# Performance work log

Measured on AMD Instinct MI355X. Metric: run time of the kernel, lower is better.

Reference implementation:

```python
import jax, jax.numpy as jnp
import numpy as np
from jax import lax

B, S, I, H = 256, 2048, 32, 18


def setup_inputs() -> dict:
    key = jax.random.key(0)
    ks = jax.random.split(key, 40)
    d = {}
    d['input'] = jax.random.normal(ks[0], (B, S, I), jnp.float32)
    d['hidden'] = jnp.zeros((3, B, H), jnp.float32)
    ki = 1
    sc = 1.0 / np.sqrt(H)
    for l in range(3):
        in_dim = I if l == 0 else H
        d[f'Wih{l}'] = jax.random.uniform(ks[ki], (H, in_dim), jnp.float32, -sc, sc); ki += 1
        d[f'bih{l}'] = jax.random.uniform(ks[ki], (H,), jnp.float32, -sc, sc); ki += 1
        d[f'Whh{l}'] = jax.random.uniform(ks[ki], (H, H), jnp.float32, -sc, sc); ki += 1
        d[f'bhh{l}'] = jax.random.uniform(ks[ki], (H,), jnp.float32, -sc, sc); ki += 1
    dims = [(H, H), (10, H), (8, 10), (4, 8), (2, 4), (1, 2)]
    for i, (o, ii) in enumerate(dims, start=1):
        s = 1.0 / np.sqrt(ii)
        d[f'W{i}'] = jax.random.uniform(ks[ki], (o, ii), jnp.float32, -s, s); ki += 1
        d[f'b{i}'] = jax.random.uniform(ks[ki], (o,), jnp.float32, -s, s); ki += 1
    return d


def _rnn_layer(x, h0, Wih, bih, Whh, bhh):
    # Precompute input contributions for all timesteps (one big GEMM),
    # then scan only the tiny hxh recurrence.
    xW = jnp.einsum('bsi,hi->bsh', x, Wih) + bih + bhh  # [B,S,H]

    def step(h, xw_t):
        h = jnp.tanh(xw_t + h @ Whh.T)
        return h, h

    hT, ys = lax.scan(step, h0, jnp.swapaxes(xW, 0, 1))  # scan over time
    return jnp.swapaxes(ys, 0, 1), hT


def reference(input, hidden,
              Wih0, bih0, Whh0, bhh0,
              Wih1, bih1, Whh1, bhh1,
              Wih2, bih2, Whh2, bhh2,
              W1, b1, W2, b2, W3, b3, W4, b4, W5, b5, W6, b6):
    layer_params = [(Wih0, bih0, Whh0, bhh0),
                    (Wih1, bih1, Whh1, bhh1),
                    (Wih2, bih2, Whh2, bhh2)]
    x = input
    h_finals = []
    for l, (Wih, bih, Whh, bhh) in enumerate(layer_params):
        x, hT = _rnn_layer(x, hidden[l], Wih, bih, Whh, bhh)
        h_finals.append(hT)
    hidden_out = jnp.stack(h_finals)  # [3,B,H]

    b_, s_, h_ = x.shape
    o = x.reshape(-1, h_)
    for W, b in [(W1, b1), (W2, b2), (W3, b3), (W4, b4), (W5, b5)]:
        o = jax.nn.relu(o @ W.T + b)
    o = o @ W6.T + b6
    return o.reshape(b_, s_, -1), hidden_out
```

## Files before the change

kernel.cpp:

```cpp
#include <hip/hip_runtime.h>

#define Bsz 256
#define Ssz 2048
#define Isz 32
#define Hsz 18
#define SCALE 2.885390081777927f

typedef float f2 __attribute__((ext_vector_type(2)));
typedef float f4 __attribute__((ext_vector_type(4)));

#define LO2(v) __builtin_shufflevector(v, v, 0, 1)
#define HI2(v) __builtin_shufflevector(v, v, 2, 3)

__device__ __forceinline__ float exp2_fast(float x) {
#if __has_builtin(__builtin_amdgcn_exp2f)
    return __builtin_amdgcn_exp2f(x);
#else
    return __expf(x * 0.6931471805599453f);
#endif
}

__global__ __launch_bounds__(256) void input_gemm(
    const float* __restrict__ x,
    const float* __restrict__ Wih0,
    const float* __restrict__ bih0,
    const float* __restrict__ bhh0,
    float* __restrict__ xw0T)
{
    __shared__ float xs[256 * 33];
    int blk = blockIdx.x;
    int b = blk >> 3;
    int t0 = (blk & 7) << 8;
    int tid = threadIdx.x;

    const float4* src = (const float4*)(x + ((size_t)b * Ssz + t0) * Isz);
#pragma unroll
    for (int k = 0; k < 8; ++k) {
        int l = k * 256 + tid;
        float4 v = src[l];
        int row = l >> 3, k4 = l & 7;
        float* p = xs + row * 33 + k4 * 4;
        p[0] = v.x; p[1] = v.y; p[2] = v.z; p[3] = v.w;
    }
    __syncthreads();

    float xv[32];
    const float* myrow = xs + tid * 33;
#pragma unroll
    for (int k = 0; k < 32; ++k) xv[k] = myrow[k];

    float* op = xw0T + (size_t)b * (Hsz * Ssz) + (t0 + tid);
#pragma unroll
    for (int ii = 0; ii < Hsz; ++ii) {
        float acc = bih0[ii] + bhh0[ii];
#pragma unroll
        for (int k = 0; k < 32; ++k) acc = fmaf(xv[k], Wih0[ii * Isz + k], acc);
        op[(size_t)ii * Ssz] = acc * SCALE;
    }
}

__global__ __launch_bounds__(64) void rnn_scan(
    const float* __restrict__ xw0T,
    const float* __restrict__ hidden,
    const float* __restrict__ Whh0,
    const float* __restrict__ Wih1, const float* __restrict__ bih1,
    const float* __restrict__ Whh1, const float* __restrict__ bhh1,
    const float* __restrict__ Wih2, const float* __restrict__ bih2,
    const float* __restrict__ Whh2, const float* __restrict__ bhh2,
    float* __restrict__ h2T,
    float* __restrict__ hid_out)
{
    const int b = blockIdx.x;
    const int r = threadIdx.x;
    const int g = (r < 18) ? 0 : (r < 36) ? 1 : (r < 54) ? 2 : 3;
    const int i = r - g * 18;
    const bool lane_active = (g < 3);
    const bool g0lane = (g == 0);
    const bool g2lane = (g == 2);

    __shared__ __align__(16) float sbuf[176];
    for (int k = r; k < 176; k += 64) sbuf[k] = 0.0f;

    float wx[Hsz], wh[Hsz];
    float econst = 0.0f;
    float h = 0.0f;
    if (lane_active) {
        const float* Whh = (g == 0) ? Whh0 : (g == 1) ? Whh1 : Whh2;
#pragma unroll
        for (int j = 0; j < Hsz; ++j) wh[j] = Whh[i * Hsz + j] * SCALE;
        if (g >= 1) {
            const float* Wih = (g == 1) ? Wih1 : Wih2;
            const float* bi  = (g == 1) ? bih1 : bih2;
            const float* bh  = (g == 1) ? bhh1 : bhh2;
#pragma unroll
            for (int j = 0; j < Hsz; ++j) wx[j] = Wih[i * Hsz + j] * SCALE;
            econst = (bi[i] + bh[i]) * SCALE;
        } else {
#pragma unroll
            for (int j = 0; j < Hsz; ++j) wx[j] = 0.0f;
        }
        h = hidden[(g * Bsz + b) * Hsz + i];
    } else {
#pragma unroll
        for (int j = 0; j < Hsz; ++j) { wx[j] = 0.0f; wh[j] = 0.0f; }
    }

    f2 wx2[9], wh2[9];
#pragma unroll
    for (int k = 0; k < 9; ++k) {
        wx2[k] = f2{wx[2 * k], wx[2 * k + 1]};
        wh2[k] = f2{wh[2 * k], wh[2 * k + 1]};
    }

    const int slot  = 36 + 36 * g + i;
    const int xbase = 36 * g;
    const int hbase = 36 * g + 36;

    sbuf[slot] = h;
    __builtin_amdgcn_wave_barrier();

    const float* xwp = xw0T + (size_t)b * (Hsz * Ssz) + (size_t)((g == 0) ? i : 0) * Ssz;
    float*       hop2 = h2T + (size_t)b * (Hsz * Ssz) + (size_t)i * Ssz;

    const f4* sx4 = (const f4*)(sbuf + xbase);
    const f4* sh4 = (const f4*)(sbuf + hbase);
    const f2* sx2 = (const f2*)(sbuf + xbase + 16);
    const f2* sh2 = (const f2*)(sbuf + hbase + 16);

    f4 cur = *(const f4*)(xwp + 0);
    f4 nxt = *(const f4*)(xwp + 4);
    f4 ob;

    auto do_tick = [&](float e, bool dostore, int st) -> float {
        f4 qa = sx4[0], qb = sx4[1], qc = sx4[2], qd = sx4[3];
        f2 qe = sx2[0];
        f4 pa = sh4[0], pb = sh4[1], pc = sh4[2], pd = sh4[3];
        f2 pe = sh2[0];
        if (dostore && g2lane) *(f4*)(hop2 + st) = ob;
        f2 ax0 = f2{e, 0.0f}, ax1 = f2{0.0f, 0.0f}, ax2 = f2{0.0f, 0.0f};
        f2 ah0 = f2{0.0f, 0.0f}, ah1 = f2{0.0f, 0.0f}, ah2 = f2{0.0f, 0.0f};
        ax0 = __builtin_elementwise_fma(wx2[0], LO2(qa), ax0);
        ax1 = __builtin_elementwise_fma(wx2[1], HI2(qa), ax1);
        ax2 = __builtin_elementwise_fma(wx2[2], LO2(qb), ax2);
        ah0 = __builtin_elementwise_fma(wh2[0], LO2(pa), ah0);
        ah1 = __builtin_elementwise_fma(wh2[1], HI2(pa), ah1);
        ah2 = __builtin_elementwise_fma(wh2[2], LO2(pb), ah2);
        ax0 = __builtin_elementwise_fma(wx2[3], HI2(qb), ax0);
        ax1 = __builtin_elementwise_fma(wx2[4], LO2(qc), ax1);
        ax2 = __builtin_elementwise_fma(wx2[5], HI2(qc), ax2);
        ah0 = __builtin_elementwise_fma(wh2[3], HI2(pb), ah0);
        ah1 = __builtin_elementwise_fma(wh2[4], LO2(pc), ah1);
        ah2 = __builtin_elementwise_fma(wh2[5], HI2(pc), ah2);
        ax0 = __builtin_elementwise_fma(wx2[6], LO2(qd), ax0);
        ax1 = __builtin_elementwise_fma(wx2[7], HI2(qd), ax1);
        ax2 = __builtin_elementwise_fma(wx2[8], qe,      ax2);
        ah0 = __builtin_elementwise_fma(wh2[6], LO2(pd), ah0);
        ah1 = __builtin_elementwise_fma(wh2[7], HI2(pd), ah1);
        ah2 = __builtin_elementwise_fma(wh2[8], pe,      ah2);
        f2 t0 = ax0 + ax1, t1 = ax2 + ah0, t2 = ah1 + ah2;
        f2 s = (t0 + t1) + t2;
        float a = s.x + s.y;
        float t = exp2_fast(a);
        return fmaf(-2.0f, __builtin_amdgcn_rcpf(t + 1.0f), 1.0f);
    };

    {
        f4 fut = *(const f4*)(xwp + 8);
        float ev[4] = {cur.x, cur.y, cur.z, cur.w};
#pragma unroll
        for (int u = 0; u < 4; ++u) {
            const int T = u;
            float e = g0lane ? ev[u] : econst;
            float nh = do_tick(e, false, 0);
            bool upd = lane_active && (T >= g);
            h = upd ? nh : h;
            sbuf[slot] = h;
            if (u == 2) ob.x = h; else if (u == 3) ob.y = h;
            __builtin_amdgcn_wave_barrier();
        }
        cur = nxt; nxt = fut;
    }

    for (int tb = 4; tb < Ssz; tb += 4) {
        int tl = tb + 8; if (tl > Ssz - 4) tl = Ssz - 4;
        f4 fut = *(const f4*)(xwp + tl);
        float ev[4] = {cur.x, cur.y, cur.z, cur.w};
#pragma unroll
        for (int u = 0; u < 4; ++u) {
            float e = g0lane ? ev[u] : econst;
            h = do_tick(e, u == 2, tb - 4);
            sbuf[slot] = h;
            if (u == 0) ob.z = h;
            else if (u == 1) ob.w = h;
            else if (u == 2) ob.x = h;
            else ob.y = h;
            __builtin_amdgcn_wave_barrier();
        }
        cur = nxt; nxt = fut;
    }

    {
        float ev[4] = {cur.x, cur.y, cur.z, cur.w};
#pragma unroll
        for (int u = 0; u < 2; ++u) {
            const int T = Ssz + u;
            float e = g0lane ? ev[u] : econst;
            float nh = do_tick(e, false, 0);
            bool upd = lane_active && (T <= Ssz - 1 + g);
            h = upd ? nh : h;
            sbuf[slot] = h;
            if (u == 0) ob.z = h; else ob.w = h;
            __builtin_amdgcn_wave_barrier();
        }
        if (g2lane) *(f4*)(hop2 + Ssz - 4) = ob;
    }

    if (lane_active) hid_out[(g * Bsz + b) * Hsz + i] = h;
}

__global__ __launch_bounds__(256) void mlp_head(
    const float* __restrict__ h2T,
    const float* __restrict__ W1, const float* __restrict__ b1,
    const float* __restrict__ W2, const float* __restrict__ b2,
    const float* __restrict__ W3, const float* __restrict__ b3,
    const float* __restrict__ W4, const float* __restrict__ b4,
    const float* __restrict__ W5, const float* __restrict__ b5,
    const float* __restrict__ W6, const float* __restrict__ b6,
    float* __restrict__ out)
{
    int idx = blockIdx.x * 256 + threadIdx.x;
    int b = idx >> 11;
    int t = idx & (Ssz - 1);
    const float* hp = h2T + (size_t)b * (Hsz * Ssz) + t;
    float v[Hsz];
#pragma unroll
    for (int j = 0; j < Hsz; ++j) v[j] = hp[(size_t)j * Ssz];

    float a1[18];
#pragma unroll
    for (int o = 0; o < 18; ++o) {
        float acc = b1[o];
#pragma unroll
        for (int j = 0; j < 18; ++j) acc = fmaf(W1[o * 18 + j], v[j], acc);
        a1[o] = fmaxf(acc, 0.0f);
    }
    float a2[10];
#pragma unroll
    for (int o = 0; o < 10; ++o) {
        float acc = b2[o];
#pragma unroll
        for (int j = 0; j < 18; ++j) acc = fmaf(W2[o * 18 + j], a1[j], acc);
        a2[o] = fmaxf(acc, 0.0f);
    }
    float a3[8];
#pragma unroll
    for (int o = 0; o < 8; ++o) {
        float acc = b3[o];
#pragma unroll
        for (int j = 0; j < 10; ++j) acc = fmaf(W3[o * 10 + j], a2[j], acc);
        a3[o] = fmaxf(acc, 0.0f);
    }
    float a4[4];
#pragma unroll
    for (int o = 0; o < 4; ++o) {
        float acc = b4[o];
#pragma unroll
        for (int j = 0; j < 8; ++j) acc = fmaf(W4[o * 8 + j], a3[j], acc);
        a4[o] = fmaxf(acc, 0.0f);
    }
    float a5[2];
#pragma unroll
    for (int o = 0; o < 2; ++o) {
        float acc = b5[o];
#pragma unroll
        for (int j = 0; j < 4; ++j) acc = fmaf(W5[o * 4 + j], a4[j], acc);
        a5[o] = fmaxf(acc, 0.0f);
    }
    float r6 = b6[0];
    r6 = fmaf(W6[0], a5[0], r6);
    r6 = fmaf(W6[1], a5[1], r6);
    out[idx] = r6;
}

extern "C" void kernel_launch(void* const* d_in, const int* in_sizes, int n_in,
                              void* d_out, int out_size, void* d_ws, size_t ws_size,
                              hipStream_t stream) {
    (void)in_sizes; (void)n_in; (void)out_size; (void)ws_size;
    const float* input  = (const float*)d_in[0];
    const float* hidden = (const float*)d_in[1];
    const float* Wih0 = (const float*)d_in[2];  const float* bih0 = (const float*)d_in[3];
    const float* Whh0 = (const float*)d_in[4];  const float* bhh0 = (const float*)d_in[5];
    const float* Wih1 = (const float*)d_in[6];  const float* bih1 = (const float*)d_in[7];
    const float* Whh1 = (const float*)d_in[8];  const float* bhh1 = (const float*)d_in[9];
    const float* Wih2 = (const float*)d_in[10]; const float* bih2 = (const float*)d_in[11];
    const float* Whh2 = (const float*)d_in[12]; const float* bhh2 = (const float*)d_in[13];
    const float* W1 = (const float*)d_in[14]; const float* b1 = (const float*)d_in[15];
    const float* W2 = (const float*)d_in[16]; const float* b2 = (const float*)d_in[17];
    const float* W3 = (const float*)d_in[18]; const float* b3 = (const float*)d_in[19];
    const float* W4 = (const float*)d_in[20]; const float* b4 = (const float*)d_in[21];
    const float* W5 = (const float*)d_in[22]; const float* b5 = (const float*)d_in[23];
    const float* W6 = (const float*)d_in[24]; const float* b6 = (const float*)d_in[25];

    float* xw0T = (float*)d_ws;
    float* h2T  = xw0T + (size_t)Bsz * Hsz * Ssz;
    float* out  = (float*)d_out;
    float* hout = out + (size_t)Bsz * Ssz;

    input_gemm<<<dim3(2048), dim3(256), 0, stream>>>(input, Wih0, bih0, bhh0, xw0T);
    rnn_scan<<<dim3(256), dim3(64), 0, stream>>>(xw0T, hidden, Whh0,
                                                 Wih1, bih1, Whh1, bhh1,
                                                 Wih2, bih2, Whh2, bhh2,
                                                 h2T, hout);
    mlp_head<<<dim3(2048), dim3(256), 0, stream>>>(h2T, W1, b1, W2, b2, W3, b3,
                                                   W4, b4, W5, b5, W6, b6, out);
}
```

Measured before the change: 441.3 us.

## Process two batch sequences per wave in RNN scan to interleave recurrences

Each rnn_scan block now advances two independent batch elements in lockstep, with separate shared-memory state buffers and interleaved dot-product/tanh chains, and the grid is halved to 128 blocks. The intent is to hide the per-step LDS and transcendental latency of the serial recurrence with a second independent chain. The cost is more instructions per step and only half as many waves in flight, leaving many CUs idle.

New measurement: 642.5 us. 45.6% more time.

```diff
diff --git a/kernel.cpp b/kernel.cpp
--- a/kernel.cpp
+++ b/kernel.cpp
@@ -70,7 +70,8 @@
     float* __restrict__ h2T,
     float* __restrict__ hid_out)
 {
-    const int b = blockIdx.x;
+    const int bp = blockIdx.x;
+    const int b0 = bp * 2, b1 = b0 + 1;
     const int r = threadIdx.x;
     const int g = (r < 18) ? 0 : (r < 36) ? 1 : (r < 54) ? 2 : 3;
     const int i = r - g * 18;
@@ -78,12 +79,14 @@
     const bool g0lane = (g == 0);
     const bool g2lane = (g == 2);
 
-    __shared__ __align__(16) float sbuf[176];
-    for (int k = r; k < 176; k += 64) sbuf[k] = 0.0f;
+    __shared__ __align__(16) float sbuf[384];
+    for (int k = r; k < 384; k += 64) sbuf[k] = 0.0f;
+    float* sbufA = sbuf;
+    float* sbufB = sbuf + 192;
 
     float wx[Hsz], wh[Hsz];
     float econst = 0.0f;
-    float h = 0.0f;
+    float hA = 0.0f, hB = 0.0f;
     if (lane_active) {
         const float* Whh = (g == 0) ? Whh0 : (g == 1) ? Whh1 : Whh2;
 #pragma unroll
@@ -99,7 +102,8 @@
 #pragma unroll
             for (int j = 0; j < Hsz; ++j) wx[j] = 0.0f;
         }
-        h = hidden[(g * Bsz + b) * Hsz + i];
+        hA = hidden[(g * Bsz + b0) * Hsz + i];
+        hB = hidden[(g * Bsz + b1) * Hsz + i];
     } else {
 #pragma unroll
         for (int j = 0; j < Hsz; ++j) { wx[j] = 0.0f; wh[j] = 0.0f; }
@@ -116,27 +120,30 @@
     const int xbase = 36 * g;
     const int hbase = 36 * g + 36;
 
-    sbuf[slot] = h;
+    sbufA[slot] = hA;
+    sbufB[slot] = hB;
     __builtin_amdgcn_wave_barrier();
 
-    const float* xwp = xw0T + (size_t)b * (Hsz * Ssz) + (size_t)((g == 0) ? i : 0) * Ssz;
-    float*       hop2 = h2T + (size_t)b * (Hsz * Ssz) + (size_t)i * Ssz;
-
-    const f4* sx4 = (const f4*)(sbuf + xbase);
-    const f4* sh4 = (const f4*)(sbuf + hbase);
-    const f2* sx2 = (const f2*)(sbuf + xbase + 16);
-    const f2* sh2 = (const f2*)(sbuf + hbase + 16);
-
-    f4 cur = *(const f4*)(xwp + 0);
-    f4 nxt = *(const f4*)(xwp + 4);
-    f4 ob;
-
-    auto do_tick = [&](float e, bool dostore, int st) -> float {
-        f4 qa = sx4[0], qb = sx4[1], qc = sx4[2], qd = sx4[3];
-        f2 qe = sx2[0];
-        f4 pa = sh4[0], pb = sh4[1], pc = sh4[2], pd = sh4[3];
-        f2 pe = sh2[0];
-        if (dostore && g2lane) *(f4*)(hop2 + st) = ob;
+    const float* xwpA = xw0T + (size_t)b0 * (Hsz * Ssz) + (size_t)((g == 0) ? i : 0) * Ssz;
+    const float* xwpB = xw0T + (size_t)b1 * (Hsz * Ssz) + (size_t)((g == 0) ? i : 0) * Ssz;
+    float*       hopA = h2T + (size_t)b0 * (Hsz * Ssz) + (size_t)i * Ssz;
+    float*       hopB = h2T + (size_t)b1 * (Hsz * Ssz) + (size_t)i * Ssz;
+
+    const f4* sx4A = (const f4*)(sbufA + xbase);
+    const f4* sh4A = (const f4*)(sbufA + hbase);
+    const f2* sx2A = (const f2*)(sbufA + xbase + 16);
+    const f2* sh2A = (const f2*)(sbufA + hbase + 16);
+    const f4* sx4B = (const f4*)(sbufB + xbase);
+    const f4* sh4B = (const f4*)(sbufB + hbase);
+    const f2* sx2B = (const f2*)(sbufB + xbase + 16);
+    const f2* sh2B = (const f2*)(sbufB + hbase + 16);
+
+    f4 curA = *(const f4*)(xwpA + 0), nxtA = *(const f4*)(xwpA + 4);
+    f4 curB = *(const f4*)(xwpB + 0), nxtB = *(const f4*)(xwpB + 4);
+    f4 obA, obB;
+
+    auto dot_tanh = [&](float e, f4 qa, f4 qb, f4 qc, f4 qd, f2 qe,
+                                 f4 pa, f4 pb, f4 pc, f4 pd, f2 pe) -> float {
         f2 ax0 = f2{e, 0.0f}, ax1 = f2{0.0f, 0.0f}, ax2 = f2{0.0f, 0.0f};
         f2 ah0 = f2{0.0f, 0.0f}, ah1 = f2{0.0f, 0.0f}, ah2 = f2{0.0f, 0.0f};
         ax0 = __builtin_elementwise_fma(wx2[0], LO2(qa), ax0);
@@ -164,58 +171,91 @@
         return fmaf(-2.0f, __builtin_amdgcn_rcpf(t + 1.0f), 1.0f);
     };
 
+    auto do_tick = [&](float eA, float eB, bool use_mask, bool upd,
+                       bool dostore, int st) {
+        f4 qa0 = sx4A[0], qb0 = sx4A[1], qc0 = sx4A[2], qd0 = sx4A[3];
+        f2 qe0 = sx2A[0];
+        f4 pa0 = sh4A[0], pb0 = sh4A[1], pc0 = sh4A[2], pd0 = sh4A[3];
+        f2 pe0 = sh2A[0];
+        f4 qa1 = sx4B[0], qb1 = sx4B[1], qc1 = sx4B[2], qd1 = sx4B[3];
+        f2 qe1 = sx2B[0];
+        f4 pa1 = sh4B[0], pb1 = sh4B[1], pc1 = sh4B[2], pd1 = sh4B[3];
+        f2 pe1 = sh2B[0];
+        if (dostore && g2lane) {
+            *(f4*)(hopA + st) = obA;
+            *(f4*)(hopB + st) = obB;
+        }
+        float nhA = dot_tanh(eA, qa0, qb0, qc0, qd0, qe0, pa0, pb0, pc0, pd0, pe0);
+        hA = use_mask ? (upd ? nhA : hA) : nhA;
+        sbufA[slot] = hA;
+        float nhB = dot_tanh(eB, qa1, qb1, qc1, qd1, qe1, pa1, pb1, pc1, pd1, pe1);
+        hB = use_mask ? (upd ? nhB : hB) : nhB;
+        sbufB[slot] = hB;
+        __builtin_amdgcn_wave_barrier();
+    };
+
     {
-        f4 fut = *(const f4*)(xwp + 8);
-        float ev[4] = {cur.x, cur.y, cur.z, cur.w};
+        f4 futA = *(const f4*)(xwpA + 8);
+        f4 futB = *(const f4*)(xwpB + 8);
+        float evA[4] = {curA.x, curA.y, curA.z, curA.w};
+        float evB[4] = {curB.x, curB.y, curB.z, curB.w};
 #pragma unroll
         for (int u = 0; u < 4; ++u) {
             const int T = u;
-            float e = g0lane ? ev[u] : econst;
-            float nh = do_tick(e, false, 0);
+            float eA = g0lane ? evA[u] : econst;
+            float eB = g0lane ? evB[u] : econst;
             bool upd = lane_active && (T >= g);
-            h = upd ? nh : h;
-            sbuf[slot] = h;
-            if (u == 2) ob.x = h; else if (u == 3) ob.y = h;
-            __builtin_amdgcn_wave_barrier();
-        }
-        cur = nxt; nxt = fut;
+            do_tick(eA, eB, true, upd, false, 0);
+            if (u == 2) { obA.x = hA; obB.x = hB; }
+            else if (u == 3) { obA.y = hA; obB.y = hB; }
+        }
+        curA = nxtA; nxtA = futA;
+        curB = nxtB; nxtB = futB;
     }
 
     for (int tb = 4; tb < Ssz; tb += 4) {
         int tl = tb + 8; if (tl > Ssz - 4) tl = Ssz - 4;
-        f4 fut = *(const f4*)(xwp + tl);
-        float ev[4] = {cur.x, cur.y, cur.z, cur.w};
+        f4 futA = *(const f4*)(xwpA + tl);
+        f4 futB = *(const f4*)(xwpB + tl);
+        float evA[4] = {curA.x, curA.y, curA.z, curA.w};
+        float evB[4] = {curB.x, curB.y, curB.z, curB.w};
 #pragma unroll
         for (int u = 0; u < 4; ++u) {
-            float e = g0lane ? ev[u] : econst;
-            h = do_tick(e, u == 2, tb - 4);
-            sbuf[slot] = h;
-            if (u == 0) ob.z = h;
-            else if (u == 1) ob.w = h;
-            else if (u == 2) ob.x = h;
-            else ob.y = h;
-            __builtin_amdgcn_wave_barrier();
-        }
-        cur = nxt; nxt = fut;
+            float eA = g0lane ? evA[u] : econst;
+            float eB = g0lane ? evB[u] : econst;
+            do_tick(eA, eB, false, false, u == 2, tb - 4);
+            if (u == 0)      { obA.z = hA; obB.z = hB; }
+            else if (u == 1) { obA.w = hA; obB.w = hB; }
+            else if (u == 2) { obA.x = hA; obB.x = hB; }
+            else             { obA.y = hA; obB.y = hB; }
+        }
+        curA = nxtA; nxtA = futA;
+        curB = nxtB; nxtB = futB;
     }
 
     {
-        float ev[4] = {cur.x, cur.y, cur.z, cur.w};
+        float evA[4] = {curA.x, curA.y, curA.z, curA.w};
+        float evB[4] = {curB.x, curB.y, curB.z, curB.w};
 #pragma unroll
         for (int u = 0; u < 2; ++u) {
             const int T = Ssz + u;
-            float e = g0lane ? ev[u] : econst;
-            float nh = do_tick(e, false, 0);
+            float eA = g0lane ? evA[u] : econst;
+            float eB = g0lane ? evB[u] : econst;
             bool upd = lane_active && (T <= Ssz - 1 + g);
-            h = upd ? nh : h;
-            sbuf[slot] = h;
-            if (u == 0) ob.z = h; else ob.w = h;
-            __builtin_amdgcn_wave_barrier();
-        }
-        if (g2lane) *(f4*)(hop2 + Ssz - 4) = ob;
-    }
-
-    if (lane_active) hid_out[(g * Bsz + b) * Hsz + i] = h;
+            do_tick(eA, eB, true, upd, false, 0);
+            if (u == 0) { obA.z = hA; obB.z = hB; }
+            else        { obA.w = hA; obB.w = hB; }
+        }
+        if (g2lane) {
+            *(f4*)(hopA + Ssz - 4) = obA;
+            *(f4*)(hopB + Ssz - 4) = obB;
+        }
+    }
+
+    if (lane_active) {
+        hid_out[(g * Bsz + b0) * Hsz + i] = hA;
+        hid_out[(g * Bsz + b1) * Hsz + i] = hB;
+    }
 }
 
 __global__ __launch_bounds__(256) void mlp_head(
@@ -307,7 +347,7 @@
     float* hout = out + (size_t)Bsz * Ssz;
 
     input_gemm<<<dim3(2048), dim3(256), 0, stream>>>(input, Wih0, bih0, bhh0, xw0T);
-    rnn_scan<<<dim3(256), dim3(64), 0, stream>>>(xw0T, hidden, Whh0,
+    rnn_scan<<<dim3(128), dim3(64), 0, stream>>>(xw0T, hidden, Whh0,
                                                  Wih1, bih1, Whh1, bhh1,
                                                  Wih2, bih2, Whh2, bhh2,
                                                  h2T, hout);
```
